# Kernel optimization log

Hardware: AMD Instinct MI355X
Metric: run time of the kernel (lower is better)

Reference implementation:

```python
import jax, jax.numpy as jnp
import numpy as np

D_MODEL = 512
N_HEADS = 8
D_K = 64
D_V = 64
SEQ = 2048
BATCH = 4
WINDOW = 256  # mask_lenth
LN_EPS = 1e-5


def setup_inputs() -> dict:
    key = jax.random.key(0)
    ks = jax.random.split(key, 7)
    s = 1.0 / np.sqrt(D_MODEL)
    return {
        "input_Q": jax.random.normal(ks[0], (BATCH, SEQ, D_MODEL), jnp.float32),
        "input_K": jax.random.normal(ks[1], (BATCH, SEQ, D_MODEL), jnp.float32),
        "input_V": jax.random.normal(ks[2], (BATCH, SEQ, D_MODEL), jnp.float32),
        "W_Q": jax.random.normal(ks[3], (D_MODEL, N_HEADS * D_K), jnp.float32) * s,
        "W_K": jax.random.normal(ks[4], (D_MODEL, N_HEADS * D_K), jnp.float32) * s,
        "W_V": jax.random.normal(ks[5], (D_MODEL, N_HEADS * D_V), jnp.float32) * s,
        "W_fc": jax.random.normal(ks[6], (N_HEADS * D_V, D_MODEL), jnp.float32) * s,
    }


def _band_mask(n, w):
    # keep entries with i-(w-1) <= j <= i  (lower band of width w incl. diagonal)
    i = jnp.arange(n)[:, None]
    j = jnp.arange(n)[None, :]
    return (j <= i) & (j >= i - (w - 1))


def reference(input_Q, input_K, input_V, W_Q, W_K, W_V, W_fc):
    B, L, _ = input_Q.shape
    # projections -> [B, H, L, d]
    Q = (input_Q @ W_Q).reshape(B, L, N_HEADS, D_K).transpose(0, 2, 1, 3)
    K = (input_K @ W_K).reshape(B, L, N_HEADS, D_K).transpose(0, 2, 1, 3)
    V = (input_V @ W_V).reshape(B, L, N_HEADS, D_V).transpose(0, 2, 1, 3)

    scores = jnp.einsum("bhqd,bhkd->bhqk", Q, K) / np.sqrt(D_K)
    mask = _band_mask(L, WINDOW)  # [L, L] bool
    scores = jnp.where(mask[None, None], scores, -jnp.inf)
    attn = jax.nn.softmax(scores, axis=-1)
    context = jnp.einsum("bhqk,bhkd->bhqd", attn, V)  # [B,H,L,d_v]
    context = context.transpose(0, 2, 1, 3).reshape(B, L, N_HEADS * D_V)
    out = context @ W_fc + input_Q  # residual
    # LayerNorm (fresh nn.LayerNorm: gamma=1, beta=0)
    mu = jnp.mean(out, axis=-1, keepdims=True)
    var = jnp.var(out, axis=-1, keepdims=True)
    return (out - mu) * jax.lax.rsqrt(var + LN_EPS)
```

## Files before the change

kernel.cpp:

```cpp
#include <hip/hip_runtime.h>
#include <hip/hip_bf16.h>

#define D_MODEL 512
#define NH      8
#define SEQ     2048
#define BATCH   4
#define WINDOW  256
#define ROWS    (BATCH*SEQ)

typedef __attribute__((ext_vector_type(8))) short bf16x8;
typedef __attribute__((ext_vector_type(4))) float f32x4;
typedef __hip_bfloat16 bf16;

__device__ __forceinline__ f32x4 mfma16(bf16x8 a, bf16x8 b, f32x4 c) {
    return __builtin_amdgcn_mfma_f32_16x16x32_bf16(a, b, c, 0, 0, 0);
}

__device__ __forceinline__ void gload16(const void* g, void* l) {
    __builtin_amdgcn_global_load_lds((const __attribute__((address_space(1))) void*)g,
                                     (__attribute__((address_space(3))) void*)l, 16, 0, 0);
}

__device__ __forceinline__ unsigned f2bf_u(float f) {
    bf16 h = __float2bfloat16(f);
    return (unsigned)(*(unsigned short*)&h);
}

__device__ __forceinline__ unsigned pack2(float lo, float hi) {
    float2 t; t.x = lo; t.y = hi;
    __hip_bfloat162 h = __float22bfloat162_rn(t);
    return *(unsigned*)&h;
}

__global__ __launch_bounds__(256)
void wconv(const float* __restrict__ W0, const float* __restrict__ W1,
           const float* __restrict__ W2, const float* __restrict__ W3,
           bf16* __restrict__ Wt) {
    const int z = blockIdx.z;
    const float* W = (z == 0) ? W0 : (z == 1) ? W1 : (z == 2) ? W2 : W3;
    bf16* dst = Wt + (size_t)z * D_MODEL * D_MODEL;

    __shared__ float t[64][65];
    const int k0 = blockIdx.x * 64, n0 = blockIdx.y * 64;
    const int tid = threadIdx.x;

    #pragma unroll
    for (int i = 0; i < 16; ++i) {
        const int e = tid + 256 * i, r = e >> 6, c = e & 63;
        t[r][c] = W[(size_t)(k0 + r) * D_MODEL + n0 + c];
    }
    __syncthreads();
    #pragma unroll
    for (int i = 0; i < 16; ++i) {
        const int e = tid + 256 * i, r = e >> 6, c = e & 63;
        dst[(size_t)(n0 + r) * D_MODEL + k0 + c] = __float2bfloat16(t[c][r]);
    }
}

__global__ __launch_bounds__(256)
void proj_mfma(const float* __restrict__ Xq, const float* __restrict__ Xk,
               const float* __restrict__ Xv, const bf16* __restrict__ Wt,
               bf16* __restrict__ Qp, bf16* __restrict__ Kp, bf16* __restrict__ Vp) {
    const int z = blockIdx.z;
    const float* X = (z == 0) ? Xq : (z == 1) ? Xk : Xv;
    const bf16* W = Wt + (size_t)z * D_MODEL * D_MODEL;
    bf16* outp = (z == 0) ? Qp : (z == 1) ? Kp : Vp;

    __shared__ bf16 Asw[2][128 * 64];
    __shared__ bf16 Bsw[2][128 * 64];

    const int tid = threadIdx.x;
    const int lane = tid & 63, w = tid >> 6;
    const int wr = w >> 1, wc = w & 1;
    const int row0 = blockIdx.x * 128, col0 = blockIdx.y * 128;
    const int g = lane >> 4, m16 = lane & 15;

    f32x4 acc[4][4] = {};
    float4 a0[4], a1[4];

    auto stageB = [&](int buf, int k0) {
        #pragma unroll
        for (int i = 0; i < 4; ++i) {
            const int chunk = i * 256 + w * 64 + lane;
            const int n = chunk >> 3, s = chunk & 7;
            gload16(W + (size_t)(col0 + n) * D_MODEL + k0 + ((s ^ (n & 7)) * 8),
                    &Bsw[buf][(i * 256 + w * 64) * 8]);
        }
    };
    auto loadA = [&](int k0) {
        #pragma unroll
        for (int i = 0; i < 4; ++i) {
            const int chunk = i * 256 + tid;
            const int m = chunk >> 3, s = chunk & 7;
            const float* gp = X + (size_t)(row0 + m) * D_MODEL + k0 + ((s ^ (m & 7)) * 8);
            a0[i] = *(const float4*)gp;
            a1[i] = *(const float4*)(gp + 4);
        }
    };
    auto writeA = [&](int buf) {
        #pragma unroll
        for (int i = 0; i < 4; ++i) {
            const int chunk = i * 256 + tid;
            const int m = chunk >> 3, s = chunk & 7;
            int4 pk;
            pk.x = pack2(a0[i].x, a0[i].y);
            pk.y = pack2(a0[i].z, a0[i].w);
            pk.z = pack2(a1[i].x, a1[i].y);
            pk.w = pack2(a1[i].z, a1[i].w);
            *(int4*)&Asw[buf][m * 64 + s * 8] = pk;
        }
    };

    stageB(0, 0);
    loadA(0);
    writeA(0);
    __syncthreads();

    int cur = 0;
    for (int step = 0; step < 8; ++step) {
        const int k0n = (step + 1) * 64;
        if (step < 7) { stageB(cur ^ 1, k0n); loadA(k0n); }

        #pragma unroll
        for (int c = 0; c < 2; ++c) {
            bf16x8 af[4], bfr[4];
            #pragma unroll
            for (int mi = 0; mi < 4; ++mi) {
                const int m = wr * 64 + mi * 16 + m16;
                const int slot = (c * 4 + g) ^ (m & 7);
                af[mi] = *(const bf16x8*)&Asw[cur][m * 64 + slot * 8];
            }
            #pragma unroll
            for (int ni = 0; ni < 4; ++ni) {
                const int n = wc * 64 + ni * 16 + m16;
                const int slot = (c * 4 + g) ^ (n & 7);
                bfr[ni] = *(const bf16x8*)&Bsw[cur][n * 64 + slot * 8];
            }
            #pragma unroll
            for (int mi = 0; mi < 4; ++mi)
                #pragma unroll
                for (int ni = 0; ni < 4; ++ni)
                    acc[mi][ni] = mfma16(af[mi], bfr[ni], acc[mi][ni]);
        }

        if (step < 7) {
            writeA(cur ^ 1);
            __syncthreads();
        }
        cur ^= 1;
    }

    if (z < 2) {
        #pragma unroll
        for (int mi = 0; mi < 4; ++mi)
            #pragma unroll
            for (int ni = 0; ni < 4; ++ni) {
                const int c = col0 + wc * 64 + ni * 16 + m16;
                const int h = c >> 6, d = c & 63;
                #pragma unroll
                for (int reg = 0; reg < 4; ++reg) {
                    const int r = row0 + wr * 64 + mi * 16 + g * 4 + reg;
                    const int b = r >> 11, l = r & (SEQ - 1);
                    outp[(((size_t)b * NH + h) * SEQ + l) * 64 + d] =
                        __float2bfloat16(acc[mi][ni][reg]);
                }
            }
    } else {
        #pragma unroll
        for (int mi = 0; mi < 4; ++mi)
            #pragma unroll
            for (int ni = 0; ni < 4; ++ni) {
                const int c = col0 + wc * 64 + ni * 16 + m16;
                const int h = c >> 6, d = c & 63;
                const int r = row0 + wr * 64 + mi * 16 + g * 4;
                const int b = r >> 11, l = r & (SEQ - 1);
                uint2 pv;
                pv.x = f2bf_u(acc[mi][ni][0]) | (f2bf_u(acc[mi][ni][1]) << 16);
                pv.y = f2bf_u(acc[mi][ni][2]) | (f2bf_u(acc[mi][ni][3]) << 16);
                *(uint2*)&outp[(((size_t)b * NH + h) * 64 + d) * SEQ + l] = pv;
            }
    }
}

__global__ __launch_bounds__(256)
void attn_mfma(const bf16* __restrict__ Qp, const bf16* __restrict__ Kp,
               const bf16* __restrict__ Vp, bf16* __restrict__ ctx) {
    __shared__ bf16 Qs[64 * 64];
    __shared__ bf16 Ks[2][64 * 64];
    __shared__ bf16 Vt[2][64 * 64];
    __shared__ bf16 Ps[4][16 * 64];

    const int bh = blockIdx.y, b = bh >> 3, h = bh & 7;
    const int q0 = blockIdx.x * 64;
    const int tid = threadIdx.x;
    const int lane = tid & 63, w = tid >> 6;
    const int g = lane >> 4, m16 = lane & 15;

    const size_t kvbase = (size_t)bh * SEQ * 64;
    const size_t vtbase = (size_t)bh * 64 * SEQ;

    auto stageKV = [&](int buf, int k0) {
        #pragma unroll
        for (int i = 0; i < 2; ++i) {
            const int chunk = i * 256 + tid;
            const int r = chunk >> 3, s = chunk & 7;
            gload16(Kp + kvbase + (size_t)(k0 + r) * 64 + ((s ^ (r & 7)) * 8),
                    &Ks[buf][(i * 256 + w * 64) * 8]);
            gload16(Vp + vtbase + (size_t)r * SEQ + k0 + ((s ^ (r & 7)) * 8),
                    &Vt[buf][(i * 256 + w * 64) * 8]);
        }
    };

    int klo = q0 - (WINDOW - 1); if (klo < 0) klo = 0;
    const int kt0 = klo >> 6, kt1 = q0 >> 6;

    #pragma unroll
    for (int i = 0; i < 2; ++i) {
        const int chunk = i * 256 + tid;
        const int r = chunk >> 3, s = chunk & 7;
        gload16(Qp + kvbase + (size_t)(q0 + r) * 64 + ((s ^ (r & 7)) * 8),
                &Qs[(i * 256 + w * 64) * 8]);
    }
    stageKV(0, kt0 * 64);
    __syncthreads();

    bf16x8 qf[2];
    #pragma unroll
    for (int c = 0; c < 2; ++c) {
        const int r = w * 16 + m16;
        qf[c] = *(const bf16x8*)&Qs[r * 64 + (((c * 4 + g) ^ (m16 & 7)) * 8)];
    }

    f32x4 o[4] = {};
    float rs = 0.f;
    const int qg = q0 + w * 16 + m16;

    int cur = 0;
    for (int kt = kt0; kt <= kt1; ++kt) {
        const int k0 = kt * 64;
        if (kt < kt1) stageKV(cur ^ 1, (kt + 1) * 64);

        f32x4 st[4] = {};
        #pragma unroll
        for (int c = 0; c < 2; ++c) {
            bf16x8 kf[4];
            #pragma unroll
            for (int f = 0; f < 4; ++f) {
                const int r = f * 16 + m16;
                kf[f] = *(const bf16x8*)&Ks[cur][r * 64 + (((c * 4 + g) ^ (m16 & 7)) * 8)];
            }
            #pragma unroll
            for (int f = 0; f < 4; ++f)
                st[f] = mfma16(kf[f], qf[c], st[f]);
        }

        const int masktype = (k0 == q0) ? 1 : ((k0 < q0 - 192) ? 2 : 0);
        #pragma unroll
        for (int f = 0; f < 4; ++f) {
            float p[4];
            #pragma unroll
            for (int reg = 0; reg < 4; ++reg) {
                const int kg = k0 + f * 16 + g * 4 + reg;
                bool valid = (masktype == 0) || (masktype == 1 ? (kg <= qg)
                                                              : (kg >= qg - (WINDOW - 1)));
                p[reg] = valid ? __expf(st[f][reg] * 0.125f) : 0.f;
                rs += p[reg];
            }
            uint2 pkv;
            pkv.x = pack2(p[0], p[1]);
            pkv.y = pack2(p[2], p[3]);
            const int slot = (f * 2 + (g >> 1)) ^ (m16 & 7);
            *(uint2*)&Ps[w][m16 * 64 + slot * 8 + (g & 1) * 4] = pkv;
        }

        #pragma unroll
        for (int c = 0; c < 2; ++c) {
            const bf16x8 pf =
                *(const bf16x8*)&Ps[w][m16 * 64 + (((c * 4 + g) ^ (m16 & 7)) * 8)];
            #pragma unroll
            for (int f2 = 0; f2 < 4; ++f2) {
                const int r = f2 * 16 + m16;
                const bf16x8 vf =
                    *(const bf16x8*)&Vt[cur][r * 64 + (((c * 4 + g) ^ (m16 & 7)) * 8)];
                o[f2] = mfma16(pf, vf, o[f2]);
            }
        }

        if (kt < kt1) __syncthreads();
        cur ^= 1;
    }

    rs += __shfl_xor(rs, 16, 64);
    rs += __shfl_xor(rs, 32, 64);
    const float inv = 1.0f / rs;
    float invr[4];
    #pragma unroll
    for (int reg = 0; reg < 4; ++reg)
        invr[reg] = __shfl(inv, g * 4 + reg, 64);

    #pragma unroll
    for (int f2 = 0; f2 < 4; ++f2) {
        const int d = f2 * 16 + m16;
        #pragma unroll
        for (int reg = 0; reg < 4; ++reg) {
            const int qrow = w * 16 + g * 4 + reg;
            ctx[((size_t)b * SEQ + q0 + qrow) * D_MODEL + h * 64 + d] =
                __float2bfloat16(o[f2][reg] * invr[reg]);
        }
    }
}

__global__ __launch_bounds__(256)
void fc_mfma(const bf16* __restrict__ ctx, const bf16* __restrict__ Wt,
             const float* __restrict__ resid, float* __restrict__ out) {
    __shared__ bf16 Asw[2][128 * 64];
    __shared__ bf16 Bsw[2][128 * 64];

    const int tid = threadIdx.x;
    const int lane = tid & 63, w = tid >> 6;
    const int wr = w >> 1, wc = w & 1;
    const int row0 = blockIdx.x * 128, col0 = blockIdx.y * 128;
    const int g = lane >> 4, m16 = lane & 15;

    f32x4 acc[4][4] = {};

    auto stage = [&](int buf, int k0) {
        #pragma unroll
        for (int i = 0; i < 4; ++i) {
            const int chunk = i * 256 + w * 64 + lane;
            const int m = chunk >> 3, s = chunk & 7;
            gload16(ctx + (size_t)(row0 + m) * D_MODEL + k0 + ((s ^ (m & 7)) * 8),
                    &Asw[buf][(i * 256 + w * 64) * 8]);
            gload16(Wt + (size_t)(col0 + m) * D_MODEL + k0 + ((s ^ (m & 7)) * 8),
                    &Bsw[buf][(i * 256 + w * 64) * 8]);
        }
    };

    stage(0, 0);
    __syncthreads();

    int cur = 0;
    for (int step = 0; step < 8; ++step) {
        if (step < 7) stage(cur ^ 1, (step + 1) * 64);

        #pragma unroll
        for (int c = 0; c < 2; ++c) {
            bf16x8 af[4], bfr[4];
            #pragma unroll
            for (int mi = 0; mi < 4; ++mi) {
                const int m = wr * 64 + mi * 16 + m16;
                const int slot = (c * 4 + g) ^ (m & 7);
                af[mi] = *(const bf16x8*)&Asw[cur][m * 64 + slot * 8];
            }
            #pragma unroll
            for (int ni = 0; ni < 4; ++ni) {
                const int n = wc * 64 + ni * 16 + m16;
                const int slot = (c * 4 + g) ^ (n & 7);
                bfr[ni] = *(const bf16x8*)&Bsw[cur][n * 64 + slot * 8];
            }
            #pragma unroll
            for (int mi = 0; mi < 4; ++mi)
                #pragma unroll
                for (int ni = 0; ni < 4; ++ni)
                    acc[mi][ni] = mfma16(af[mi], bfr[ni], acc[mi][ni]);
        }

        if (step < 7) __syncthreads();
        cur ^= 1;
    }

    #pragma unroll
    for (int mi = 0; mi < 4; ++mi)
        #pragma unroll
        for (int ni = 0; ni < 4; ++ni) {
            const int c = col0 + wc * 64 + ni * 16 + m16;
            #pragma unroll
            for (int reg = 0; reg < 4; ++reg) {
                const int r = row0 + wr * 64 + mi * 16 + g * 4 + reg;
                out[(size_t)r * D_MODEL + c] = acc[mi][ni][reg] + resid[(size_t)r * D_MODEL + c];
            }
        }
}

__global__ __launch_bounds__(256)
void ln_kernel(float* __restrict__ out) {
    const int row = blockIdx.x;
    float* p = out + (size_t)row * D_MODEL;
    const int tid = threadIdx.x;

    float2 x = *(float2*)&p[tid * 2];
    float s  = x.x + x.y;
    float s2 = x.x * x.x + x.y * x.y;
    #pragma unroll
    for (int m = 1; m < 64; m <<= 1) {
        s  += __shfl_xor(s,  m, 64);
        s2 += __shfl_xor(s2, m, 64);
    }
    __shared__ float sa[4], sb[4];
    const int w = tid >> 6;
    if ((tid & 63) == 0) { sa[w] = s; sb[w] = s2; }
    __syncthreads();
    s  = sa[0] + sa[1] + sa[2] + sa[3];
    s2 = sb[0] + sb[1] + sb[2] + sb[3];

    const float mean = s * (1.0f / D_MODEL);
    const float var  = s2 * (1.0f / D_MODEL) - mean * mean;
    const float rstd = rsqrtf(var + 1e-5f);

    x.x = (x.x - mean) * rstd;
    x.y = (x.y - mean) * rstd;
    *(float2*)&p[tid * 2] = x;
}

extern "C" void kernel_launch(void* const* d_in, const int* in_sizes, int n_in,
                              void* d_out, int out_size, void* d_ws, size_t ws_size,
                              hipStream_t stream) {
    const float* inQ = (const float*)d_in[0];
    const float* inK = (const float*)d_in[1];
    const float* inV = (const float*)d_in[2];
    const float* WQ  = (const float*)d_in[3];
    const float* WK  = (const float*)d_in[4];
    const float* WV  = (const float*)d_in[5];
    const float* Wfc = (const float*)d_in[6];
    float* out = (float*)d_out;

    bf16* ws = (bf16*)d_ws;
    const size_t WSZ = (size_t)D_MODEL * D_MODEL;
    const size_t NE  = (size_t)BATCH * NH * SEQ * 64;
    bf16* Wt   = ws;
    bf16* Qp   = ws + 4 * WSZ;
    bf16* Kp   = Qp + NE;
    bf16* Vp   = Kp + NE;
    bf16* ctxb = Vp + NE;

    wconv<<<dim3(8, 8, 4), 256, 0, stream>>>(WQ, WK, WV, Wfc, Wt);
    proj_mfma<<<dim3(ROWS / 128, D_MODEL / 128, 3), 256, 0, stream>>>(
        inQ, inK, inV, Wt, Qp, Kp, Vp);
    attn_mfma<<<dim3(SEQ / 64, BATCH * NH), 256, 0, stream>>>(Qp, Kp, Vp, ctxb);
    fc_mfma<<<dim3(ROWS / 128, D_MODEL / 128), 256, 0, stream>>>(
        ctxb, Wt + 3 * WSZ, inQ, out);
    ln_kernel<<<ROWS, 256, 0, stream>>>(out);
}
```

Baseline: 177.7 us.

## Shrink GEMM tiles to 64x64 and read attention K/V directly from global

The projection and output-FC GEMMs move from 128x128 to 64x64 block tiles, giving four times as many blocks and using less LDS per block, which should help occupancy. The attention kernel drops its shared-memory staging of Q, K and V and the block-wide barriers. Each wave now reads its operands straight from global memory, and each wave computes its own key-tile range and mask from its 16-row query slice. The risk is lower data reuse in the GEMMs and uncoalesced, cache-dependent global loads in attention.

Result: slower. 192.6 us (+8.4%).

```diff
diff --git a/kernel.cpp b/kernel.cpp
--- a/kernel.cpp
+++ b/kernel.cpp
@@ -66,21 +66,21 @@
     const bf16* W = Wt + (size_t)z * D_MODEL * D_MODEL;
     bf16* outp = (z == 0) ? Qp : (z == 1) ? Kp : Vp;
 
-    __shared__ bf16 Asw[2][128 * 64];
-    __shared__ bf16 Bsw[2][128 * 64];
+    __shared__ bf16 Asw[2][64 * 64];
+    __shared__ bf16 Bsw[2][64 * 64];
 
     const int tid = threadIdx.x;
     const int lane = tid & 63, w = tid >> 6;
     const int wr = w >> 1, wc = w & 1;
-    const int row0 = blockIdx.x * 128, col0 = blockIdx.y * 128;
+    const int row0 = blockIdx.x * 64, col0 = blockIdx.y * 64;
     const int g = lane >> 4, m16 = lane & 15;
 
-    f32x4 acc[4][4] = {};
-    float4 a0[4], a1[4];
+    f32x4 acc[2][2] = {};
+    float4 a0[2], a1[2];
 
     auto stageB = [&](int buf, int k0) {
         #pragma unroll
-        for (int i = 0; i < 4; ++i) {
+        for (int i = 0; i < 2; ++i) {
             const int chunk = i * 256 + w * 64 + lane;
             const int n = chunk >> 3, s = chunk & 7;
             gload16(W + (size_t)(col0 + n) * D_MODEL + k0 + ((s ^ (n & 7)) * 8),
@@ -89,7 +89,7 @@
     };
     auto loadA = [&](int k0) {
         #pragma unroll
-        for (int i = 0; i < 4; ++i) {
+        for (int i = 0; i < 2; ++i) {
             const int chunk = i * 256 + tid;
             const int m = chunk >> 3, s = chunk & 7;
             const float* gp = X + (size_t)(row0 + m) * D_MODEL + k0 + ((s ^ (m & 7)) * 8);
@@ -99,7 +99,7 @@
     };
     auto writeA = [&](int buf) {
         #pragma unroll
-        for (int i = 0; i < 4; ++i) {
+        for (int i = 0; i < 2; ++i) {
             const int chunk = i * 256 + tid;
             const int m = chunk >> 3, s = chunk & 7;
             int4 pk;
@@ -123,23 +123,23 @@
 
         #pragma unroll
         for (int c = 0; c < 2; ++c) {
-            bf16x8 af[4], bfr[4];
-            #pragma unroll
-            for (int mi = 0; mi < 4; ++mi) {
-                const int m = wr * 64 + mi * 16 + m16;
+            bf16x8 af[2], bfr[2];
+            #pragma unroll
+            for (int mi = 0; mi < 2; ++mi) {
+                const int m = wr * 32 + mi * 16 + m16;
                 const int slot = (c * 4 + g) ^ (m & 7);
                 af[mi] = *(const bf16x8*)&Asw[cur][m * 64 + slot * 8];
             }
             #pragma unroll
-            for (int ni = 0; ni < 4; ++ni) {
-                const int n = wc * 64 + ni * 16 + m16;
+            for (int ni = 0; ni < 2; ++ni) {
+                const int n = wc * 32 + ni * 16 + m16;
                 const int slot = (c * 4 + g) ^ (n & 7);
                 bfr[ni] = *(const bf16x8*)&Bsw[cur][n * 64 + slot * 8];
             }
             #pragma unroll
-            for (int mi = 0; mi < 4; ++mi)
+            for (int mi = 0; mi < 2; ++mi)
                 #pragma unroll
-                for (int ni = 0; ni < 4; ++ni)
+                for (int ni = 0; ni < 2; ++ni)
                     acc[mi][ni] = mfma16(af[mi], bfr[ni], acc[mi][ni]);
         }
 
@@ -152,14 +152,14 @@
 
     if (z < 2) {
         #pragma unroll
-        for (int mi = 0; mi < 4; ++mi)
-            #pragma unroll
-            for (int ni = 0; ni < 4; ++ni) {
-                const int c = col0 + wc * 64 + ni * 16 + m16;
+        for (int mi = 0; mi < 2; ++mi)
+            #pragma unroll
+            for (int ni = 0; ni < 2; ++ni) {
+                const int c = col0 + wc * 32 + ni * 16 + m16;
                 const int h = c >> 6, d = c & 63;
                 #pragma unroll
                 for (int reg = 0; reg < 4; ++reg) {
-                    const int r = row0 + wr * 64 + mi * 16 + g * 4 + reg;
+                    const int r = row0 + wr * 32 + mi * 16 + g * 4 + reg;
                     const int b = r >> 11, l = r & (SEQ - 1);
                     outp[(((size_t)b * NH + h) * SEQ + l) * 64 + d] =
                         __float2bfloat16(acc[mi][ni][reg]);
@@ -167,16 +167,16 @@
             }
     } else {
         #pragma unroll
-        for (int mi = 0; mi < 4; ++mi)
-            #pragma unroll
-            for (int ni = 0; ni < 4; ++ni) {
-                const int c = col0 + wc * 64 + ni * 16 + m16;
+        for (int mi = 0; mi < 2; ++mi)
+            #pragma unroll
+            for (int ni = 0; ni < 2; ++ni) {
+                const int c = col0 + wc * 32 + ni * 16 + m16;
                 const int h = c >> 6, d = c & 63;
-                const int r = row0 + wr * 64 + mi * 16 + g * 4;
+                const int r = row0 + wr * 32 + mi * 16 + g * 4;
                 const int b = r >> 11, l = r & (SEQ - 1);
                 uint2 pv;
-                pv.x = f2bf_u(acc[mi][ni][0]) | (f2bf_u(acc[mi][ni][1]) << 16);
-                pv.y = f2bf_u(acc[mi][ni][2]) | (f2bf_u(acc[mi][ni][3]) << 16);
+                pv.x = pack2(acc[mi][ni][0], acc[mi][ni][1]);
+                pv.y = pack2(acc[mi][ni][2], acc[mi][ni][3]);
                 *(uint2*)&outp[(((size_t)b * NH + h) * 64 + d) * SEQ + l] = pv;
             }
     }
@@ -185,76 +185,46 @@
 __global__ __launch_bounds__(256)
 void attn_mfma(const bf16* __restrict__ Qp, const bf16* __restrict__ Kp,
                const bf16* __restrict__ Vp, bf16* __restrict__ ctx) {
-    __shared__ bf16 Qs[64 * 64];
-    __shared__ bf16 Ks[2][64 * 64];
-    __shared__ bf16 Vt[2][64 * 64];
     __shared__ bf16 Ps[4][16 * 64];
 
     const int bh = blockIdx.y, b = bh >> 3, h = bh & 7;
-    const int q0 = blockIdx.x * 64;
     const int tid = threadIdx.x;
     const int lane = tid & 63, w = tid >> 6;
     const int g = lane >> 4, m16 = lane & 15;
+    const int q0w = blockIdx.x * 64 + w * 16;
 
     const size_t kvbase = (size_t)bh * SEQ * 64;
     const size_t vtbase = (size_t)bh * 64 * SEQ;
 
-    auto stageKV = [&](int buf, int k0) {
-        #pragma unroll
-        for (int i = 0; i < 2; ++i) {
-            const int chunk = i * 256 + tid;
-            const int r = chunk >> 3, s = chunk & 7;
-            gload16(Kp + kvbase + (size_t)(k0 + r) * 64 + ((s ^ (r & 7)) * 8),
-                    &Ks[buf][(i * 256 + w * 64) * 8]);
-            gload16(Vp + vtbase + (size_t)r * SEQ + k0 + ((s ^ (r & 7)) * 8),
-                    &Vt[buf][(i * 256 + w * 64) * 8]);
-        }
-    };
-
-    int klo = q0 - (WINDOW - 1); if (klo < 0) klo = 0;
-    const int kt0 = klo >> 6, kt1 = q0 >> 6;
-
-    #pragma unroll
-    for (int i = 0; i < 2; ++i) {
-        const int chunk = i * 256 + tid;
-        const int r = chunk >> 3, s = chunk & 7;
-        gload16(Qp + kvbase + (size_t)(q0 + r) * 64 + ((s ^ (r & 7)) * 8),
-                &Qs[(i * 256 + w * 64) * 8]);
-    }
-    stageKV(0, kt0 * 64);
-    __syncthreads();
-
     bf16x8 qf[2];
     #pragma unroll
-    for (int c = 0; c < 2; ++c) {
-        const int r = w * 16 + m16;
-        qf[c] = *(const bf16x8*)&Qs[r * 64 + (((c * 4 + g) ^ (m16 & 7)) * 8)];
-    }
+    for (int c = 0; c < 2; ++c)
+        qf[c] = *(const bf16x8*)(Qp + kvbase + (size_t)(q0w + m16) * 64 + c * 32 + g * 8);
 
     f32x4 o[4] = {};
     float rs = 0.f;
-    const int qg = q0 + w * 16 + m16;
-
-    int cur = 0;
+    const int qg = q0w + m16;
+
+    int klo = q0w - (WINDOW - 1); if (klo < 0) klo = 0;
+    const int kt0 = klo >> 6, kt1 = q0w >> 6;
+
     for (int kt = kt0; kt <= kt1; ++kt) {
         const int k0 = kt * 64;
-        if (kt < kt1) stageKV(cur ^ 1, (kt + 1) * 64);
 
         f32x4 st[4] = {};
         #pragma unroll
         for (int c = 0; c < 2; ++c) {
             bf16x8 kf[4];
             #pragma unroll
-            for (int f = 0; f < 4; ++f) {
-                const int r = f * 16 + m16;
-                kf[f] = *(const bf16x8*)&Ks[cur][r * 64 + (((c * 4 + g) ^ (m16 & 7)) * 8)];
-            }
+            for (int f = 0; f < 4; ++f)
+                kf[f] = *(const bf16x8*)(Kp + kvbase +
+                         (size_t)(k0 + f * 16 + m16) * 64 + c * 32 + g * 8);
             #pragma unroll
             for (int f = 0; f < 4; ++f)
                 st[f] = mfma16(kf[f], qf[c], st[f]);
         }
 
-        const int masktype = (k0 == q0) ? 1 : ((k0 < q0 - 192) ? 2 : 0);
+        const int masktype = (kt == kt1) ? 1 : ((k0 < q0w - 240) ? 2 : 0);
         #pragma unroll
         for (int f = 0; f < 4; ++f) {
             float p[4];
@@ -279,15 +249,11 @@
                 *(const bf16x8*)&Ps[w][m16 * 64 + (((c * 4 + g) ^ (m16 & 7)) * 8)];
             #pragma unroll
             for (int f2 = 0; f2 < 4; ++f2) {
-                const int r = f2 * 16 + m16;
-                const bf16x8 vf =
-                    *(const bf16x8*)&Vt[cur][r * 64 + (((c * 4 + g) ^ (m16 & 7)) * 8)];
+                const bf16x8 vf = *(const bf16x8*)(Vp + vtbase +
+                         (size_t)(f2 * 16 + m16) * SEQ + k0 + c * 32 + g * 8);
                 o[f2] = mfma16(pf, vf, o[f2]);
             }
         }
-
-        if (kt < kt1) __syncthreads();
-        cur ^= 1;
     }
 
     rs += __shfl_xor(rs, 16, 64);
@@ -303,8 +269,8 @@
         const int d = f2 * 16 + m16;
         #pragma unroll
         for (int reg = 0; reg < 4; ++reg) {
-            const int qrow = w * 16 + g * 4 + reg;
-            ctx[((size_t)b * SEQ + q0 + qrow) * D_MODEL + h * 64 + d] =
+            const int qrow = q0w + g * 4 + reg;
+            ctx[((size_t)b * SEQ + qrow) * D_MODEL + h * 64 + d] =
                 __float2bfloat16(o[f2][reg] * invr[reg]);
         }
     }
@@ -313,20 +279,20 @@
 __global__ __launch_bounds__(256)
 void fc_mfma(const bf16* __restrict__ ctx, const bf16* __restrict__ Wt,
              const float* __restrict__ resid, float* __restrict__ out) {
-    __shared__ bf16 Asw[2][128 * 64];
-    __shared__ bf16 Bsw[2][128 * 64];
+    __shared__ bf16 Asw[2][64 * 64];
+    __shared__ bf16 Bsw[2][64 * 64];
 
     const int tid = threadIdx.x;
     const int lane = tid & 63, w = tid >> 6;
     const int wr = w >> 1, wc = w & 1;
-    const int row0 = blockIdx.x * 128, col0 = blockIdx.y * 128;
+    const int row0 = blockIdx.x * 64, col0 = blockIdx.y * 64;
     const int g = lane >> 4, m16 = lane & 15;
 
-    f32x4 acc[4][4] = {};
+    f32x4 acc[2][2] = {};
 
     auto stage = [&](int buf, int k0) {
         #pragma unroll
-        for (int i = 0; i < 4; ++i) {
+        for (int i = 0; i < 2; ++i) {
             const int chunk = i * 256 + w * 64 + lane;
             const int m = chunk >> 3, s = chunk & 7;
             gload16(ctx + (size_t)(row0 + m) * D_MODEL + k0 + ((s ^ (m & 7)) * 8),
@@ -345,23 +311,23 @@
 
         #pragma unroll
         for (int c = 0; c < 2; ++c) {
-            bf16x8 af[4], bfr[4];
-            #pragma unroll
-            for (int mi = 0; mi < 4; ++mi) {
-                const int m = wr * 64 + mi * 16 + m16;
+            bf16x8 af[2], bfr[2];
+            #pragma unroll
+            for (int mi = 0; mi < 2; ++mi) {
+                const int m = wr * 32 + mi * 16 + m16;
                 const int slot = (c * 4 + g) ^ (m & 7);
                 af[mi] = *(const bf16x8*)&Asw[cur][m * 64 + slot * 8];
             }
             #pragma unroll
-            for (int ni = 0; ni < 4; ++ni) {
-                const int n = wc * 64 + ni * 16 + m16;
+            for (int ni = 0; ni < 2; ++ni) {
+                const int n = wc * 32 + ni * 16 + m16;
                 const int slot = (c * 4 + g) ^ (n & 7);
                 bfr[ni] = *(const bf16x8*)&Bsw[cur][n * 64 + slot * 8];
             }
             #pragma unroll
-            for (int mi = 0; mi < 4; ++mi)
+            for (int mi = 0; mi < 2; ++mi)
                 #pragma unroll
-                for (int ni = 0; ni < 4; ++ni)
+                for (int ni = 0; ni < 2; ++ni)
                     acc[mi][ni] = mfma16(af[mi], bfr[ni], acc[mi][ni]);
         }
 
@@ -370,13 +336,13 @@
     }
 
     #pragma unroll
-    for (int mi = 0; mi < 4; ++mi)
-        #pragma unroll
-        for (int ni = 0; ni < 4; ++ni) {
-            const int c = col0 + wc * 64 + ni * 16 + m16;
+    for (int mi = 0; mi < 2; ++mi)
+        #pragma unroll
+        for (int ni = 0; ni < 2; ++ni) {
+            const int c = col0 + wc * 32 + ni * 16 + m16;
             #pragma unroll
             for (int reg = 0; reg < 4; ++reg) {
-                const int r = row0 + wr * 64 + mi * 16 + g * 4 + reg;
+                const int r = row0 + wr * 32 + mi * 16 + g * 4 + reg;
                 out[(size_t)r * D_MODEL + c] = acc[mi][ni][reg] + resid[(size_t)r * D_MODEL + c];
             }
         }
@@ -434,10 +400,10 @@
     bf16* ctxb = Vp + NE;
 
     wconv<<<dim3(8, 8, 4), 256, 0, stream>>>(WQ, WK, WV, Wfc, Wt);
-    proj_mfma<<<dim3(ROWS / 128, D_MODEL / 128, 3), 256, 0, stream>>>(
+    proj_mfma<<<dim3(ROWS / 64, D_MODEL / 64, 3), 256, 0, stream>>>(
         inQ, inK, inV, Wt, Qp, Kp, Vp);
     attn_mfma<<<dim3(SEQ / 64, BATCH * NH), 256, 0, stream>>>(Qp, Kp, Vp, ctxb);
-    fc_mfma<<<dim3(ROWS / 128, D_MODEL / 128), 256, 0, stream>>>(
+    fc_mfma<<<dim3(ROWS / 64, D_MODEL / 64), 256, 0, stream>>>(
         ctxb, Wt + 3 * WSZ, inQ, out);
     ln_kernel<<<ROWS, 256, 0, stream>>>(out);
 }
```
